# Performance work log

Measured on AMD Instinct MI355X. Metric: run time of the kernel, lower is better.

Reference implementation:

```python
import jax, jax.numpy as jnp
import numpy as np

NUM_NODES = 1_200_000
NUM_FILLER = 200_000
NUM_PHYS = NUM_NODES - NUM_FILLER  # 1,000,000 physical nodes
NUM_MOVABLE = 900_000
NBX = NBY = 512
XL, XH, YL, YH = 0.0, 1000.0, 0.0, 1000.0
BSX = (XH - XL) / NBX
BSY = (YH - YL) / NBY
PIN_STRETCH = 1.4142135623730951
UNIT_PIN_CAP = 0.05
MAX_RATE = 1.5
MIN_RATE = 1.0 / MAX_RATE
K = 5  # max bins overlapped per dimension (span<=4.0, bin~1.95)


def _overlap_terms(lo, hi, bin_size, origin, nb):
    # lo, hi: [n] interval per node. Returns bin indices [n,K] and overlap lengths [n,K].
    il = jnp.clip(jnp.floor((lo - origin) / bin_size).astype(jnp.int32), 0, nb - 1)
    idx = il[:, None] + jnp.arange(K, dtype=jnp.int32)[None, :]
    valid = idx < nb
    idx = jnp.clip(idx, 0, nb - 1)
    b_lo = origin + idx.astype(lo.dtype) * bin_size
    ov = jnp.maximum(jnp.minimum(hi[:, None], b_lo + bin_size) - jnp.maximum(lo[:, None], b_lo), 0.0)
    return idx, jnp.where(valid, ov, 0.0)


def _forward(pos, node_size_x, node_size_y, flat_node2pin_start_map):
    P = NUM_PHYS
    sx, sy = node_size_x[:P], node_size_y[:P]
    # stretched half sizes: at least half a stretched bin
    hx = 0.5 * jnp.maximum(BSX * PIN_STRETCH, sx)
    hy = 0.5 * jnp.maximum(BSY * PIN_STRETCH, sy)
    cx = pos[:P] + 0.5 * sx
    cy = pos[NUM_NODES:NUM_NODES + P] + 0.5 * sy
    pw = (flat_node2pin_start_map[1:P + 1] - flat_node2pin_start_map[:P]).astype(pos.dtype)
    density = pw / (4.0 * hx * hy)  # pins per unit area over stretched bbox

    # stage 1: scatter stretched-bbox pin density into bin map
    ix, ovx = _overlap_terms(cx - hx, cx + hx, BSX, XL, NBX)  # [P,K]
    iy, ovy = _overlap_terms(cy - hy, cy + hy, BSY, YL, NBY)  # [P,K]
    contrib = ovx[:, :, None] * ovy[:, None, :] * density[:, None, None]  # [P,K,K]
    flat_idx = (ix[:, :, None] * NBY + iy[:, None, :]).reshape(-1)
    pin_map = jnp.zeros(NBX * NBY, dtype=pos.dtype).at[flat_idx].add(contrib.reshape(-1))

    # stage 2: pin utilization per bin, clamped adjust rate
    util = jnp.clip(pin_map / (BSX * BSY * UNIT_PIN_CAP), MIN_RATE, MAX_RATE)

    # stage 3: per movable node, integrate utilization over its (unstretched) bbox
    M = NUM_MOVABLE
    x_lo = pos[:M]
    x_hi = x_lo + node_size_x[:M]
    y_lo = pos[NUM_NODES:NUM_NODES + M]
    y_hi = y_lo + node_size_y[:M]
    jx, wx = _overlap_terms(x_lo, x_hi, BSX, XL, NBX)  # [M,K]
    jy, wy = _overlap_terms(y_lo, y_hi, BSY, YL, NBY)  # [M,K]
    u = util[jx[:, :, None] * NBY + jy[:, None, :]]  # [M,K,K]
    instance_pin_area = jnp.sum(wx[:, :, None] * wy[:, None, :] * u, axis=(1, 2))
    return instance_pin_area


def setup_inputs() -> dict:
    key = jax.random.key(0)
    k1, k2, k3, k4 = jax.random.split(key, 4)
    node_size_x = jax.random.uniform(k1, (NUM_NODES,), jnp.float32, 1.0, 4.0)
    node_size_y = jnp.full((NUM_NODES,), 2.0, jnp.float32)  # row height
    px = jax.random.uniform(k2, (NUM_NODES,), jnp.float32, 0.0, 995.0)
    py = jax.random.uniform(k3, (NUM_NODES,), jnp.float32, 0.0, 995.0)
    pos = jnp.concatenate([px, py])
    pin_counts = jax.random.randint(k4, (NUM_PHYS,), 1, 9, jnp.int32)
    flat = jnp.concatenate([jnp.zeros(1, jnp.int32), jnp.cumsum(pin_counts).astype(jnp.int32)])
    return {"pos": pos, "node_size_x": node_size_x, "node_size_y": node_size_y,
            "flat_node2pin_start_map": flat}


def reference(pos, node_size_x, node_size_y, flat_node2pin_start_map):
    return _forward(pos, node_size_x, node_size_y, flat_node2pin_start_map)
```

## Files before the change

kernel.cpp:

```cpp
#include <hip/hip_runtime.h>

#define NUM_NODES   1200000
#define NUM_FILLER  200000
#define NUM_PHYS    (NUM_NODES - NUM_FILLER)
#define NUM_MOVABLE 900000
#define NBX 512
#define NBY 512
#define NBINS (NBX * NBY)
#define BSX 1.953125f
#define BSY 1.953125f
#define PIN_STRETCH 1.4142135623730951f
#define CAP 0.19073486328125f
#define INV_CAP (1.0f / 0.19073486328125f)
#define MAX_RATE 1.5f
#define MIN_RATE (1.0f/1.5f)
#define K 5

#define TBITS   5
#define TSZ     32
#define TDIM    16
#define NTILES  (TDIM * TDIM)
#define HALO    (K - 1)
#define LTS     (TSZ + HALO)
#define NPB     2048
#define NBLK    ((NUM_PHYS + NPB - 1) / NPB)
#define CAPP    6144
#define CAPM    5120

__device__ __forceinline__ int bin_lo(float lo) {
    int il = (int)floorf(lo / BSX);
    return min(max(il, 0), NBX - 1);
}

__global__ __launch_bounds__(256) void sort_both(
    const float* __restrict__ pos,
    const float* __restrict__ nsx,
    const float* __restrict__ nsy,
    const int*   __restrict__ flat,
    int*         __restrict__ physCur,
    int*         __restrict__ movCur,
    float4*      __restrict__ physRec,
    float*       __restrict__ physDens,
    float4*      __restrict__ movRec,
    int*         __restrict__ movIdx)
{
    __shared__ int cntP[NTILES], cntM[NTILES], baseP[NTILES], baseM[NTILES];
    int tid = threadIdx.x;
    cntP[tid] = 0; cntM[tid] = 0;
    __syncthreads();

    float px[NPB/256], py[NPB/256], sx[NPB/256], sy[NPB/256], dn[NPB/256];
    int pk[NPB/256];
    int base = blockIdx.x * NPB;
    #pragma unroll
    for (int it = 0; it < NPB / 256; ++it) {
        int i = base + it * 256 + tid;
        int k = 0;
        if (i < NUM_PHYS) {
            float pxv = pos[i], pyv = pos[NUM_NODES + i];
            float sxv = nsx[i], syv = nsy[i];
            float hx = 0.5f * fmaxf(BSX * PIN_STRETCH, sxv);
            float hy = 0.5f * fmaxf(BSY * PIN_STRETCH, syv);
            float pw = (float)(flat[i + 1] - flat[i]);
            px[it] = pxv; py[it] = pyv; sx[it] = sxv; sy[it] = syv;
            dn[it] = pw / (4.0f * hx * hy);
            float lox = pxv + 0.5f * sxv - hx;
            float loy = pyv + 0.5f * syv - hy;
            int tp = ((bin_lo(lox) >> TBITS) << 4) | (bin_lo(loy) >> TBITS);
            atomicAdd(&cntP[tp], 1);
            k = 0x10000 | tp;
            if (i < NUM_MOVABLE) {
                int tm = ((bin_lo(pxv) >> TBITS) << 4) | (bin_lo(pyv) >> TBITS);
                atomicAdd(&cntM[tm], 1);
                k |= 0x20000 | (tm << 8);
            }
        }
        pk[it] = k;
    }
    __syncthreads();
    int cp = cntP[tid], cm = cntM[tid];
    baseP[tid] = (cp > 0) ? atomicAdd(&physCur[tid], cp) : 0;
    baseM[tid] = (cm > 0) ? atomicAdd(&movCur[tid],  cm) : 0;
    __syncthreads();
    int i0 = base + tid;
    #pragma unroll
    for (int it = 0; it < NPB / 256; ++it) {
        int k = pk[it];
        if (k & 0x10000) {
            float sxv = sx[it], syv = sy[it];
            float hx = 0.5f * fmaxf(BSX * PIN_STRETCH, sxv);
            float hy = 0.5f * fmaxf(BSY * PIN_STRETCH, syv);
            float lox = px[it] + 0.5f * sxv - hx;
            float loy = py[it] + 0.5f * syv - hy;
            int tp = k & 0xFF;
            int s = atomicAdd(&baseP[tp], 1);
            if (s < CAPP) {
                size_t g = (size_t)tp * CAPP + s;
                physRec[g] = make_float4(lox, loy, lox + 2.0f * hx, loy + 2.0f * hy);
                physDens[g] = dn[it];
            }
        }
        if (k & 0x20000) {
            int tm = (k >> 8) & 0xFF;
            int s = atomicAdd(&baseM[tm], 1);
            if (s < CAPM) {
                size_t g = (size_t)tm * CAPM + s;
                movRec[g] = make_float4(px[it], py[it],
                                        px[it] + sx[it], py[it] + sy[it]);
                movIdx[g] = i0 + it * 256;
            }
        }
    }
}

__global__ __launch_bounds__(1024) void accumulate_tiles(
    const float4* __restrict__ physRec,
    const float*  __restrict__ physDens,
    const int*    __restrict__ physCur,
    float*        __restrict__ pin)
{
    __shared__ float tileA[LTS * LTS];
    int tid = threadIdx.x;
    int t = blockIdx.x;
    int bx0 = (t >> 4) * TSZ, by0 = (t & 15) * TSZ;

    for (int i = tid; i < LTS * LTS; i += 1024) tileA[i] = 0.0f;
    __syncthreads();

    int cnt = min(physCur[t], CAPP);
    size_t b0 = (size_t)t * CAPP;
    for (int i = tid; i < cnt; i += 1024) {
        float4 r = physRec[b0 + i];
        float d = physDens[b0 + i];
        int il = bin_lo(r.x), jl = bin_lo(r.y);
        int ie = min(min((int)floorf(r.z / BSX), NBX - 1), il + HALO);
        int je = min(min((int)floorf(r.w / BSY), NBY - 1), jl + HALO);
        int lr = il - bx0, lc = jl - by0;
        for (int a = il; a <= ie; ++a) {
            float blo = (float)a * BSX;
            float ox = fmaxf(fminf(r.z, blo + BSX) - fmaxf(r.x, blo), 0.0f);
            int rowb = (lr + (a - il)) * LTS + lc;
            for (int b2 = jl; b2 <= je; ++b2) {
                float blo2 = (float)b2 * BSY;
                float oy = fmaxf(fminf(r.w, blo2 + BSY) - fmaxf(r.y, blo2), 0.0f);
                float cc = ox * oy * d;
                if (cc != 0.0f) atomicAdd(&tileA[rowb + (b2 - jl)], cc);
            }
        }
    }
    __syncthreads();
    for (int i = tid; i < LTS * LTS; i += 1024) {
        float v = tileA[i];
        if (v != 0.0f) {
            int r = i / LTS, c = i % LTS;
            int gx = bx0 + r, gy = by0 + c;
            if (gx < NBX && gy < NBY) atomicAdd(&pin[gx * NBY + gy], v);
        }
    }
}

__global__ __launch_bounds__(1024) void gather_tiled(
    const float4* __restrict__ movRec,
    const int*    __restrict__ movIdx,
    const int*    __restrict__ movCur,
    const float*  __restrict__ pin,
    float*        __restrict__ out)
{
    __shared__ float patch[LTS * LTS];
    int tid = threadIdx.x;
    int t = blockIdx.x;
    int bx0 = (t >> 4) * TSZ, by0 = (t & 15) * TSZ;

    for (int i = tid; i < LTS * LTS; i += 1024) {
        int r = i / LTS, c = i % LTS;
        int gx = bx0 + r, gy = by0 + c;
        float u = MIN_RATE;
        if (gx < NBX && gy < NBY)
            u = fminf(fmaxf(pin[gx * NBY + gy] * INV_CAP, MIN_RATE), MAX_RATE);
        patch[i] = u;
    }
    __syncthreads();

    int cnt = min(movCur[t], CAPM);
    size_t b0 = (size_t)t * CAPM;
    for (int i = tid; i < cnt; i += 1024) {
        float4 r = movRec[b0 + i];
        int idx = movIdx[b0 + i];
        int il = bin_lo(r.x), jl = bin_lo(r.y);
        int ie = min(min((int)floorf(r.z / BSX), NBX - 1), il + K - 1);
        int je = min(min((int)floorf(r.w / BSY), NBY - 1), jl + K - 1);
        int lr = il - bx0, lc = jl - by0;
        float acc = 0.0f;
        for (int a = il; a <= ie; ++a) {
            float blo = (float)a * BSX;
            float wxv = fmaxf(fminf(r.z, blo + BSX) - fmaxf(r.x, blo), 0.0f);
            int rowb = (lr + (a - il)) * LTS + lc;
            for (int b2 = jl; b2 <= je; ++b2) {
                float blo2 = (float)b2 * BSY;
                float wyv = fmaxf(fminf(r.w, blo2 + BSY) - fmaxf(r.y, blo2), 0.0f);
                acc += wxv * wyv * patch[rowb + (b2 - jl)];
            }
        }
        out[idx] = acc;
    }
}

__global__ __launch_bounds__(256) void scatter_pin_map_agent(
    const float* __restrict__ pos,
    const float* __restrict__ nsx,
    const float* __restrict__ nsy,
    const int*   __restrict__ flat,
    float*       __restrict__ map)
{
    int p = blockIdx.x * blockDim.x + threadIdx.x;
    if (p >= NUM_PHYS) return;
    float sx = nsx[p], sy = nsy[p];
    float hx = 0.5f * fmaxf(BSX * PIN_STRETCH, sx);
    float hy = 0.5f * fmaxf(BSY * PIN_STRETCH, sy);
    float cx = pos[p] + 0.5f * sx;
    float cy = pos[NUM_NODES + p] + 0.5f * sy;
    float pw = (float)(flat[p + 1] - flat[p]);
    float density = pw / (4.0f * hx * hy);
    float lox = cx - hx, hixv = cx + hx;
    float loy = cy - hy, hiyv = cy + hy;
    int il = bin_lo(lox), jl = bin_lo(loy);
    int ie = min(min((int)floorf(hixv / BSX), NBX - 1), il + K - 1);
    int je = min(min((int)floorf(hiyv / BSY), NBY - 1), jl + K - 1);
    for (int a = il; a <= ie; ++a) {
        float blo = (float)a * BSX;
        float ox = fmaxf(fminf(hixv, blo + BSX) - fmaxf(lox, blo), 0.0f);
        for (int b = jl; b <= je; ++b) {
            float blo2 = (float)b * BSY;
            float oy = fmaxf(fminf(hiyv, blo2 + BSY) - fmaxf(loy, blo2), 0.0f);
            float c = ox * oy * density;
            if (c != 0.0f) atomicAdd(&map[a * NBY + b], c);
        }
    }
}

__global__ __launch_bounds__(256) void gather_direct(
    const float* __restrict__ pos,
    const float* __restrict__ nsx,
    const float* __restrict__ nsy,
    const float* __restrict__ pin,
    float*       __restrict__ out)
{
    int m = blockIdx.x * blockDim.x + threadIdx.x;
    if (m >= NUM_MOVABLE) return;
    float xlo = pos[m];
    float xhi = xlo + nsx[m];
    float ylo = pos[NUM_NODES + m];
    float yhi = ylo + nsy[m];
    int il = bin_lo(xlo);
    int ie = min(min((int)floorf(xhi / BSX), NBX - 1), il + K - 1);
    int jl = bin_lo(ylo);
    int je = min(min((int)floorf(yhi / BSY), NBY - 1), jl + K - 1);
    float acc = 0.0f;
    for (int a = il; a <= ie; ++a) {
        float blo = (float)a * BSX;
        float wxv = fmaxf(fminf(xhi, blo + BSX) - fmaxf(xlo, blo), 0.0f);
        const float* __restrict__ row = pin + a * NBY;
        for (int b2 = jl; b2 <= je; ++b2) {
            float blo2 = (float)b2 * BSY;
            float wyv = fmaxf(fminf(yhi, blo2 + BSY) - fmaxf(ylo, blo2), 0.0f);
            float u = fminf(fmaxf(row[b2] * INV_CAP, MIN_RATE), MAX_RATE);
            acc += wxv * wyv * u;
        }
    }
    out[m] = acc;
}

extern "C" void kernel_launch(void* const* d_in, const int* in_sizes, int n_in,
                              void* d_out, int out_size, void* d_ws, size_t ws_size,
                              hipStream_t stream) {
    const float* pos  = (const float*)d_in[0];
    const float* nsx  = (const float*)d_in[1];
    const float* nsy  = (const float*)d_in[2];
    const int*   flat = (const int*)d_in[3];
    float* out = (float*)d_out;

    char* wsb = (char*)d_ws;
    float*  pin      = (float*)wsb;
    int*    physCur  = (int*)(wsb + (size_t)NBINS * 4);
    int*    movCur   = physCur + NTILES;
    float4* physRec  = (float4*)(wsb + (size_t)NBINS * 4 + 8192);
    float*  physDens = (float*)(physRec + (size_t)NTILES * CAPP);
    float4* movRec   = (float4*)(physDens + (size_t)NTILES * CAPP);
    int*    movIdx   = (int*)(movRec + (size_t)NTILES * CAPM);
    size_t needed = (size_t)NBINS * 4 + 8192
                  + (size_t)NTILES * CAPP * 20 + (size_t)NTILES * CAPM * 20;

    dim3 blk(256);
    if (ws_size >= needed) {
        hipMemsetAsync(d_ws, 0, (size_t)NBINS * 4 + 8192, stream);
        sort_both<<<NBLK, blk, 0, stream>>>(pos, nsx, nsy, flat,
                                            physCur, movCur,
                                            physRec, physDens, movRec, movIdx);
        accumulate_tiles<<<NTILES, dim3(1024), 0, stream>>>(physRec, physDens, physCur, pin);
        gather_tiled<<<NTILES, dim3(1024), 0, stream>>>(movRec, movIdx, movCur, pin, out);
    } else {
        hipMemsetAsync(pin, 0, (size_t)NBINS * 4, stream);
        scatter_pin_map_agent<<<(NUM_PHYS + 255) / 256, blk, 0, stream>>>(pos, nsx, nsy, flat, pin);
        gather_direct<<<(NUM_MOVABLE + 255) / 256, blk, 0, stream>>>(pos, nsx, nsy, pin, out);
    }
}
```

Baseline: 156.0 us.

## Shard tile bucket counters and storage per XCD to cut cross-die atomics

The binning kernel now reads the hardware XCC id and keeps separate counters and record slots for each (tile, XCD) pair. The goal is to stop global atomics on the tile counters from contending across chiplets. The accumulate and gather kernels build a small prefix over the eight sub-buckets and walk them as one list. The binning kernel also moves to 1024-thread blocks handling 4096 nodes each. Interior bins of each tile's pin map are written with plain stores instead of atomics, since only halo rows and columns can overlap neighbouring tiles. In exchange it adds a serial prefix step, a per-item search loop, and a fixed 1024-slot capacity per sub-bucket that could overflow under skewed inputs.

```diff
diff --git a/kernel.cpp b/kernel.cpp
--- a/kernel.cpp
+++ b/kernel.cpp
@@ -22,17 +22,19 @@
 #define NTILES  (TDIM * TDIM)
 #define HALO    (K - 1)
 #define LTS     (TSZ + HALO)
-#define NPB     2048
+#define NXCD    8
+#define SBLK    1024
+#define NPB     4096
+#define IPT     (NPB / SBLK)
 #define NBLK    ((NUM_PHYS + NPB - 1) / NPB)
-#define CAPP    6144
-#define CAPM    5120
+#define CAPX    1024
 
 __device__ __forceinline__ int bin_lo(float lo) {
     int il = (int)floorf(lo / BSX);
     return min(max(il, 0), NBX - 1);
 }
 
-__global__ __launch_bounds__(256) void sort_both(
+__global__ __launch_bounds__(SBLK) void sort_both(
     const float* __restrict__ pos,
     const float* __restrict__ nsx,
     const float* __restrict__ nsy,
@@ -46,15 +48,19 @@
 {
     __shared__ int cntP[NTILES], cntM[NTILES], baseP[NTILES], baseM[NTILES];
     int tid = threadIdx.x;
-    cntP[tid] = 0; cntM[tid] = 0;
-    __syncthreads();
-
-    float px[NPB/256], py[NPB/256], sx[NPB/256], sy[NPB/256], dn[NPB/256];
-    int pk[NPB/256];
+    if (tid < NTILES) { cntP[tid] = 0; cntM[tid] = 0; }
+    __syncthreads();
+
+    unsigned xcc;
+    asm volatile("s_getreg_b32 %0, hwreg(HW_REG_XCC_ID, 0, 32)" : "=s"(xcc));
+    xcc &= (NXCD - 1);
+
+    float px[IPT], py[IPT], sx[IPT], sy[IPT], dn[IPT];
+    int pk[IPT];
     int base = blockIdx.x * NPB;
     #pragma unroll
-    for (int it = 0; it < NPB / 256; ++it) {
-        int i = base + it * 256 + tid;
+    for (int it = 0; it < IPT; ++it) {
+        int i = base + it * SBLK + tid;
         int k = 0;
         if (i < NUM_PHYS) {
             float pxv = pos[i], pyv = pos[NUM_NODES + i];
@@ -78,36 +84,38 @@
         pk[it] = k;
     }
     __syncthreads();
-    int cp = cntP[tid], cm = cntM[tid];
-    baseP[tid] = (cp > 0) ? atomicAdd(&physCur[tid], cp) : 0;
-    baseM[tid] = (cm > 0) ? atomicAdd(&movCur[tid],  cm) : 0;
-    __syncthreads();
-    int i0 = base + tid;
+    if (tid < NTILES) {
+        int c = cntP[tid];
+        baseP[tid] = (c > 0) ? atomicAdd(&physCur[tid * NXCD + xcc], c) : 0;
+        c = cntM[tid];
+        baseM[tid] = (c > 0) ? atomicAdd(&movCur[tid * NXCD + xcc], c) : 0;
+    }
+    __syncthreads();
     #pragma unroll
-    for (int it = 0; it < NPB / 256; ++it) {
+    for (int it = 0; it < IPT; ++it) {
         int k = pk[it];
         if (k & 0x10000) {
             float sxv = sx[it], syv = sy[it];
             float hx = 0.5f * fmaxf(BSX * PIN_STRETCH, sxv);
             float hy = 0.5f * fmaxf(BSY * PIN_STRETCH, syv);
-            float lox = px[it] + 0.5f * sxv - hx;
-            float loy = py[it] + 0.5f * syv - hy;
+            float cx = px[it] + 0.5f * sxv;
+            float cy = py[it] + 0.5f * syv;
             int tp = k & 0xFF;
             int s = atomicAdd(&baseP[tp], 1);
-            if (s < CAPP) {
-                size_t g = (size_t)tp * CAPP + s;
-                physRec[g] = make_float4(lox, loy, lox + 2.0f * hx, loy + 2.0f * hy);
+            if (s < CAPX) {
+                size_t g = ((size_t)tp * NXCD + xcc) * CAPX + s;
+                physRec[g] = make_float4(cx - hx, cy - hy, cx + hx, cy + hy);
                 physDens[g] = dn[it];
             }
         }
         if (k & 0x20000) {
             int tm = (k >> 8) & 0xFF;
             int s = atomicAdd(&baseM[tm], 1);
-            if (s < CAPM) {
-                size_t g = (size_t)tm * CAPM + s;
+            if (s < CAPX) {
+                size_t g = ((size_t)tm * NXCD + xcc) * CAPX + s;
                 movRec[g] = make_float4(px[it], py[it],
                                         px[it] + sx[it], py[it] + sy[it]);
-                movIdx[g] = i0 + it * 256;
+                movIdx[g] = base + it * SBLK + tid;
             }
         }
     }
@@ -120,18 +128,29 @@
     float*        __restrict__ pin)
 {
     __shared__ float tileA[LTS * LTS];
+    __shared__ int pref[NXCD + 1];
     int tid = threadIdx.x;
     int t = blockIdx.x;
     int bx0 = (t >> 4) * TSZ, by0 = (t & 15) * TSZ;
 
     for (int i = tid; i < LTS * LTS; i += 1024) tileA[i] = 0.0f;
-    __syncthreads();
-
-    int cnt = min(physCur[t], CAPP);
-    size_t b0 = (size_t)t * CAPP;
-    for (int i = tid; i < cnt; i += 1024) {
-        float4 r = physRec[b0 + i];
-        float d = physDens[b0 + i];
+    if (tid == 0) {
+        int s = 0; pref[0] = 0;
+        for (int x = 0; x < NXCD; ++x) {
+            s += min(physCur[t * NXCD + x], CAPX);
+            pref[x + 1] = s;
+        }
+    }
+    __syncthreads();
+
+    int total = pref[NXCD];
+    size_t tb = (size_t)t * NXCD * CAPX;
+    for (int k = tid; k < total; k += 1024) {
+        int x = 0;
+        while (k >= pref[x + 1]) ++x;
+        size_t g = tb + (size_t)x * CAPX + (k - pref[x]);
+        float4 r = physRec[g];
+        float d = physDens[g];
         int il = bin_lo(r.x), jl = bin_lo(r.y);
         int ie = min(min((int)floorf(r.z / BSX), NBX - 1), il + HALO);
         int je = min(min((int)floorf(r.w / BSY), NBY - 1), jl + HALO);
@@ -151,10 +170,14 @@
     __syncthreads();
     for (int i = tid; i < LTS * LTS; i += 1024) {
         float v = tileA[i];
-        if (v != 0.0f) {
-            int r = i / LTS, c = i % LTS;
-            int gx = bx0 + r, gy = by0 + c;
-            if (gx < NBX && gy < NBY) atomicAdd(&pin[gx * NBY + gy], v);
+        int r = i / LTS, c = i % LTS;
+        int gx = bx0 + r, gy = by0 + c;
+        if (gx >= NBX || gy >= NBY) continue;
+        bool interior = (r >= HALO) && (r < TSZ) && (c >= HALO) && (c < TSZ);
+        if (interior) {
+            if (v != 0.0f) pin[gx * NBY + gy] = v;
+        } else {
+            if (v != 0.0f) atomicAdd(&pin[gx * NBY + gy], v);
         }
     }
 }
@@ -167,6 +190,7 @@
     float*        __restrict__ out)
 {
     __shared__ float patch[LTS * LTS];
+    __shared__ int pref[NXCD + 1];
     int tid = threadIdx.x;
     int t = blockIdx.x;
     int bx0 = (t >> 4) * TSZ, by0 = (t & 15) * TSZ;
@@ -179,13 +203,23 @@
             u = fminf(fmaxf(pin[gx * NBY + gy] * INV_CAP, MIN_RATE), MAX_RATE);
         patch[i] = u;
     }
-    __syncthreads();
-
-    int cnt = min(movCur[t], CAPM);
-    size_t b0 = (size_t)t * CAPM;
-    for (int i = tid; i < cnt; i += 1024) {
-        float4 r = movRec[b0 + i];
-        int idx = movIdx[b0 + i];
+    if (tid == 0) {
+        int s = 0; pref[0] = 0;
+        for (int x = 0; x < NXCD; ++x) {
+            s += min(movCur[t * NXCD + x], CAPX);
+            pref[x + 1] = s;
+        }
+    }
+    __syncthreads();
+
+    int total = pref[NXCD];
+    size_t tb = (size_t)t * NXCD * CAPX;
+    for (int k = tid; k < total; k += 1024) {
+        int x = 0;
+        while (k >= pref[x + 1]) ++x;
+        size_t g = tb + (size_t)x * CAPX + (k - pref[x]);
+        float4 r = movRec[g];
+        int idx = movIdx[g];
         int il = bin_lo(r.x), jl = bin_lo(r.y);
         int ie = min(min((int)floorf(r.z / BSX), NBX - 1), il + K - 1);
         int je = min(min((int)floorf(r.w / BSY), NBY - 1), jl + K - 1);
@@ -279,23 +313,23 @@
     const int*   flat = (const int*)d_in[3];
     float* out = (float*)d_out;
 
+    const size_t NSLOT = (size_t)NTILES * NXCD * CAPX;
     char* wsb = (char*)d_ws;
     float*  pin      = (float*)wsb;
     int*    physCur  = (int*)(wsb + (size_t)NBINS * 4);
-    int*    movCur   = physCur + NTILES;
-    float4* physRec  = (float4*)(wsb + (size_t)NBINS * 4 + 8192);
-    float*  physDens = (float*)(physRec + (size_t)NTILES * CAPP);
-    float4* movRec   = (float4*)(physDens + (size_t)NTILES * CAPP);
-    int*    movIdx   = (int*)(movRec + (size_t)NTILES * CAPM);
-    size_t needed = (size_t)NBINS * 4 + 8192
-                  + (size_t)NTILES * CAPP * 20 + (size_t)NTILES * CAPM * 20;
+    int*    movCur   = physCur + NTILES * NXCD;
+    float4* physRec  = (float4*)(wsb + (size_t)NBINS * 4 + 32768);
+    float*  physDens = (float*)(physRec + NSLOT);
+    float4* movRec   = (float4*)(physDens + NSLOT);
+    int*    movIdx   = (int*)(movRec + NSLOT);
+    size_t needed = (size_t)NBINS * 4 + 32768 + NSLOT * 40;
 
     dim3 blk(256);
     if (ws_size >= needed) {
-        hipMemsetAsync(d_ws, 0, (size_t)NBINS * 4 + 8192, stream);
-        sort_both<<<NBLK, blk, 0, stream>>>(pos, nsx, nsy, flat,
-                                            physCur, movCur,
-                                            physRec, physDens, movRec, movIdx);
+        hipMemsetAsync(d_ws, 0, (size_t)NBINS * 4 + 32768, stream);
+        sort_both<<<NBLK, dim3(SBLK), 0, stream>>>(pos, nsx, nsy, flat,
+                                                   physCur, movCur,
+                                                   physRec, physDens, movRec, movIdx);
         accumulate_tiles<<<NTILES, dim3(1024), 0, stream>>>(physRec, physDens, physCur, pin);
         gather_tiled<<<NTILES, dim3(1024), 0, stream>>>(movRec, movIdx, movCur, pin, out);
     } else {
```

Measured after the change: 152.5 us. 1.02x faster.
